# Kernel optimization log

Hardware: AMD Instinct MI355X
Metric: run time of the kernel (lower is better)

## Reference

```python
import jax, jax.numpy as jnp
import numpy as np

N_USER, N_NEWS = 100000, 20000
C, H, NL = 128, 4, 2
D = C // H
E = 250000
N_TYPES, N_RELS = 2, 3
EDGE_SRC_DST = ((0, 1), (1, 0), (0, 0))  # (src_type, dst_type): posts, rev_posts, follows
SIZES = (N_USER, N_NEWS)


def setup_inputs() -> dict:
    key = jax.random.key(0)
    ks = iter(jax.random.split(key, 32))
    s_lin = 1.0 / np.sqrt(C)
    s_rel = 1.0 / np.sqrt(D)
    inp = {
        "x_user": jax.random.normal(next(ks), (N_USER, C), jnp.float32),
        "x_news": jax.random.normal(next(ks), (N_NEWS, C), jnp.float32),
    }
    for name, (st, dt) in zip(("ei_posts", "ei_rev", "ei_follows"), EDGE_SRC_DST):
        src = jax.random.randint(next(ks), (E,), 0, SIZES[st], jnp.int32)
        dst = jax.random.randint(next(ks), (E,), 0, SIZES[dt], jnp.int32)
        inp[name] = jnp.stack([src, dst])  # [2, E]
    for w, b in (("Wk", "bk"), ("Wq", "bq"), ("Wv", "bv"), ("Wa", "ba")):
        inp[w] = jax.random.normal(next(ks), (NL, N_TYPES, C, C), jnp.float32) * s_lin
        inp[b] = jnp.zeros((NL, N_TYPES, C), jnp.float32)
    inp["skip"] = jnp.ones((NL, N_TYPES), jnp.float32)
    inp["a_rel"] = jax.random.normal(next(ks), (NL, N_RELS, H, D, D), jnp.float32) * s_rel
    inp["m_rel"] = jax.random.normal(next(ks), (NL, N_RELS, H, D, D), jnp.float32) * s_rel
    inp["p_rel"] = jnp.ones((NL, N_RELS, H), jnp.float32)
    return inp


def _segment_softmax(scores, seg, n):
    # scores: [E, H], seg: [E] destination ids; PyG-style softmax over incoming edges
    m = jax.ops.segment_max(scores, seg, num_segments=n)
    ex = jnp.exp(scores - m[seg])
    den = jax.ops.segment_sum(ex, seg, num_segments=n)
    return ex / (den[seg] + 1e-16)


def _hgt_layer(xs, eis, Wk, bk, Wq, bq, Wv, bv, Wa, ba, skip, a_rel, m_rel, p_rel):
    # per-node-type projections -> [N_t, H, D]
    k = [(xs[t] @ Wk[t] + bk[t]).reshape(-1, H, D) for t in range(N_TYPES)]
    q = [(xs[t] @ Wq[t] + bq[t]).reshape(-1, H, D) for t in range(N_TYPES)]
    v = [(xs[t] @ Wv[t] + bv[t]).reshape(-1, H, D) for t in range(N_TYPES)]
    agg = [jnp.zeros((SIZES[t], C), xs[t].dtype) for t in range(N_TYPES)]
    inv_sqrt_d = 1.0 / np.sqrt(D)
    for r, (st, dt) in enumerate(EDGE_SRC_DST):
        src, dst = eis[r][0], eis[r][1]
        # relation-specific transforms: W_att / W_msg per head
        k_rel = jnp.einsum('nhd,hde->nhe', k[st], a_rel[r])
        v_rel = jnp.einsum('nhd,hde->nhe', v[st], m_rel[r])
        score = jnp.einsum('ehd,ehd->eh', q[dt][dst], k_rel[src]) * p_rel[r] * inv_sqrt_d
        alpha = _segment_softmax(score, dst, SIZES[dt])  # [E, H]
        msg = (v_rel[src] * alpha[..., None]).reshape(-1, C)
        agg[dt] = agg[dt] + jax.ops.segment_sum(msg, dst, num_segments=SIZES[dt])
    new_xs = []
    for t in range(N_TYPES):
        o = jax.nn.gelu(agg[t], approximate=False) @ Wa[t] + ba[t]
        a = jax.nn.sigmoid(skip[t])
        new_xs.append(a * o + (1.0 - a) * xs[t])  # skip (dims match)
    return new_xs


def reference(x_user, x_news, ei_posts, ei_rev, ei_follows,
              Wk, bk, Wq, bq, Wv, bv, Wa, ba, skip, a_rel, m_rel, p_rel):
    xs = [x_user, x_news]
    eis = (ei_posts, ei_rev, ei_follows)
    for l in range(NL):
        xs = _hgt_layer(xs, eis, Wk[l], bk[l], Wq[l], bq[l], Wv[l], bv[l],
                        Wa[l], ba[l], skip[l], a_rel[l], m_rel[l], p_rel[l])
        xs = [jax.nn.relu(x) for x in xs]
    # x_dict output, concatenated over node types in metadata order for a single array
    return jnp.concatenate(xs, axis=0)  # [N_USER + N_NEWS, C]
```

## Files before the change

### kernel.cpp

```cpp
#include <hip/hip_runtime.h>
#include <cmath>

constexpr int NUSER = 100000;
constexpr int NNEWS = 20000;
constexpr int CH    = 128;
constexpr int NE    = 250000;
constexpr int NTOT  = NNEWS + NUSER + NUSER;
constexpr int NSB   = (NTOT + 255) / 256;

typedef _Float16 f16x8 __attribute__((ext_vector_type(8)));
typedef _Float16 f16x4 __attribute__((ext_vector_type(4)));
typedef _Float16 f16x2 __attribute__((ext_vector_type(2)));
typedef float    f32x4 __attribute__((ext_vector_type(4)));

constexpr size_t OFF_QU  = 0;
constexpr size_t OFF_QN  = OFF_QU  + (size_t)NUSER * 64;
constexpr size_t OFF_AGU = OFF_QN  + (size_t)NNEWS * 64;
constexpr size_t OFF_AGN = OFF_AGU + (size_t)NUSER * 64;
constexpr size_t OFF_KVB = OFF_AGN + (size_t)NNEWS * 64;
constexpr size_t OFF_KVS = OFF_KVB + (size_t)NUSER * 128;
constexpr size_t OFF_WF  = OFF_KVS + (size_t)NNEWS * 128;
constexpr size_t OFF_BE  = OFF_WF  + 20 * 8192;
constexpr size_t OFF_INT = OFF_BE  + 2 * 768;
constexpr size_t IO_CU   = 0;
constexpr size_t IO_JRP  = IO_CU  + NTOT;
constexpr size_t IO_BSUM = IO_JRP + NTOT + 1;
constexpr size_t IO_BOFF = IO_BSUM + NSB;
constexpr size_t IO_CL   = IO_BOFF + NSB;
constexpr size_t IO_RANK = IO_CL + 3 * NE;
constexpr size_t IO_END  = IO_RANK + 3 * NE;
constexpr size_t OFF_X16U = OFF_INT + IO_END;
constexpr size_t OFF_X16N = OFF_X16U + (size_t)NUSER * 64;
constexpr size_t OFF_KVB2 = OFF_X16N + (size_t)NNEWS * 64;
constexpr size_t WS_NEED_ROOMY = (OFF_KVB2 + (size_t)NUSER * 128) * sizeof(float);

__device__ __forceinline__ float gelu_f(float x) {
    return 0.5f * x * (1.0f + erff(x * 0.70710678118654752440f));
}

__device__ __forceinline__ int frag_dest(int k, int col) {
    int kt = k >> 5, quad = (k >> 3) & 3, j = k & 7;
    int ct = col >> 4, m = col & 15;
    int lane = quad * 16 + m;
    return ((kt * 8 + ct) * 64 + lane) * 8 + j;
}

constexpr int NEFF = 2 * 2 * 3 * 16384;
constexpr int NCVT = 2 * 4 * 16384;
constexpr int NBIA = 2 * 2 * 3 * 128;
constexpr int NPREP = NEFF + NCVT + NBIA;

__global__ __launch_bounds__(256) void prep_weights_kernel(
    const float* __restrict__ Wk, const float* __restrict__ bk,
    const float* __restrict__ Wv, const float* __restrict__ bv,
    const float* __restrict__ Wq, const float* __restrict__ Wa,
    const float* __restrict__ a_rel, const float* __restrict__ m_rel,
    const float* __restrict__ p_rel,
    _Float16* __restrict__ wkf, float* __restrict__ bke,
    _Float16* __restrict__ wvf, float* __restrict__ bve,
    _Float16* __restrict__ wqf, _Float16* __restrict__ waf,
    int* __restrict__ cu)
{
    const float kscale = 0.17677669529663688f * 1.44269504088896340f;
    int idx = blockIdx.x * 256 + threadIdx.x;
    if (idx < NEFF) {
        int o = idx & 16383;
        int g = idx >> 14;
        int r = g % 3, lk = g / 3, kind = lk & 1, l = lk >> 1;
        int st = (r == 1) ? 1 : 0;
        const float* W   = (kind ? Wv : Wk) + ((size_t)(l * 2 + st)) * 16384;
        const float* rel = (kind ? m_rel : a_rel) + ((size_t)(l * 3 + r)) * 4096;
        _Float16* Wf = (kind ? wvf : wkf) + ((size_t)(l * 3 + r)) * 16384;
        int k = o >> 7, col = o & 127, h = col >> 5, e = col & 31;
        const float* wrow = W + (size_t)k * 128 + h * 32;
        const float* rcol = rel + h * 1024 + e;
        float s = 0.f;
        #pragma unroll
        for (int d = 0; d < 32; ++d) s += wrow[d] * rcol[d * 32];
        if (kind == 0) s *= p_rel[(l * 3 + r) * 4 + h] * kscale;
        Wf[frag_dest(k, col)] = (_Float16)s;
    } else if (idx < NEFF + NCVT) {
        int t = idx - NEFF;
        int o = t & 16383;
        int b = t >> 14;
        int l = b >> 2, sub = b & 3;
        const float* W;
        _Float16* Wf;
        if (sub < 2) { W = Wq + ((size_t)(l * 2 + sub)) * 16384;     Wf = wqf + ((size_t)(l * 2 + sub)) * 16384; }
        else         { W = Wa + ((size_t)(l * 2 + sub - 2)) * 16384; Wf = waf + ((size_t)(l * 2 + sub - 2)) * 16384; }
        int k = o >> 7, col = o & 127;
        Wf[frag_dest(k, col)] = (_Float16)W[o];
    } else if (idx < NPREP) {
        int t = idx - NEFF - NCVT;
        int col = t & 127;
        int g = t >> 7;
        int r = g % 3, lk = g / 3, kind = lk & 1, l = lk >> 1;
        int st = (r == 1) ? 1 : 0;
        const float* bi  = (kind ? bv : bk) + ((size_t)(l * 2 + st)) * 128;
        const float* rel = (kind ? m_rel : a_rel) + ((size_t)(l * 3 + r)) * 4096;
        float* be = (kind ? bve : bke) + (size_t)l * 384 + r * 128;
        int h = col >> 5, e = col & 31;
        float s = 0.f;
        #pragma unroll
        for (int d = 0; d < 32; ++d) s += bi[h * 32 + d] * rel[h * 1024 + d * 32 + e];
        if (kind == 0) s *= p_rel[(l * 3 + r) * 4 + h] * kscale;
        be[col] = s;
    } else if (idx < NPREP + NTOT) {
        cu[idx - NPREP] = 0;
    }
}

__global__ void histrank_kernel(const int* __restrict__ e0, const int* __restrict__ e1,
                                const int* __restrict__ e2, int* __restrict__ cu,
                                int* __restrict__ rank) {
    int idx = blockIdx.x * 256 + threadIdx.x;
    if (idx >= 3 * NE) return;
    int r = idx / NE, e = idx - r * NE;
    const int* ei = (r == 0) ? e0 : (r == 1) ? e1 : e2;
    int base = (r == 0) ? 0 : (r == 1) ? NNEWS : (NNEWS + NUSER);
    rank[idx] = atomicAdd(&cu[base + ei[NE + e]], 1);
}

__global__ __launch_bounds__(256) void scan_part_kernel(const int* __restrict__ cu,
                                                        int* __restrict__ bsum) {
    int i = blockIdx.x * 256 + threadIdx.x;
    int v = (i < NTOT) ? cu[i] : 0;
    #pragma unroll
    for (int o = 1; o < 64; o <<= 1) v += __shfl_xor(v, o);
    __shared__ int ws_[4];
    if ((threadIdx.x & 63) == 0) ws_[threadIdx.x >> 6] = v;
    __syncthreads();
    if (threadIdx.x == 0) bsum[blockIdx.x] = ws_[0] + ws_[1] + ws_[2] + ws_[3];
}

__global__ __launch_bounds__(1024) void scan_top_kernel(const int* __restrict__ bsum,
                                                        int* __restrict__ boff,
                                                        int* __restrict__ jrp) {
    __shared__ int wsum[16];
    int tid = threadIdx.x, lane = tid & 63, w = tid >> 6;
    int v = (tid < NSB) ? bsum[tid] : 0;
    int x = v;
    #pragma unroll
    for (int o = 1; o < 64; o <<= 1) { int y = __shfl_up(x, o); if (lane >= o) x += y; }
    if (lane == 63) wsum[w] = x;
    __syncthreads();
    if (tid < 16) {
        int t = wsum[tid];
        #pragma unroll
        for (int o = 1; o < 16; o <<= 1) { int y = __shfl_up(t, o); if (tid >= o) t += y; }
        wsum[tid] = t;
    }
    __syncthreads();
    int woff = w ? wsum[w - 1] : 0;
    if (tid < NSB) boff[tid] = woff + x - v;
    if (tid == 0) jrp[NTOT] = 3 * NE;
}

__global__ __launch_bounds__(256) void scan_fin_kernel(const int* __restrict__ cu,
                                                       const int* __restrict__ boff,
                                                       int* __restrict__ jrp) {
    __shared__ int wsum[4];
    int tid = threadIdx.x, lane = tid & 63, w = tid >> 6;
    int i = blockIdx.x * 256 + tid;
    int v = (i < NTOT) ? cu[i] : 0;
    int x = v;
    #pragma unroll
    for (int o = 1; o < 64; o <<= 1) { int y = __shfl_up(x, o); if (lane >= o) x += y; }
    if (lane == 63) wsum[w] = x;
    __syncthreads();
    int woff = 0;
    #pragma unroll
    for (int k = 0; k < 4; ++k) if (k < w) woff += wsum[k];
    int excl = boff[blockIdx.x] + woff + x - v;
    if (i < NTOT) jrp[i] = excl;
}

__global__ void fill_kernel(const int* __restrict__ e0, const int* __restrict__ e1,
                            const int* __restrict__ e2, const int* __restrict__ jrp,
                            const int* __restrict__ rank, int* __restrict__ cl) {
    int idx = blockIdx.x * 256 + threadIdx.x;
    if (idx >= 3 * NE) return;
    int r = idx / NE, e = idx - r * NE;
    const int* ei = (r == 0) ? e0 : (r == 1) ? e1 : e2;
    int base = (r == 0) ? 0 : (r == 1) ? NNEWS : (NNEWS + NUSER);
    int dst = ei[NE + e], src = ei[e];
    cl[jrp[base + dst] + rank[idx]] = src;
}

struct GJob {
    const void* A;
    const _Float16* W0;
    const _Float16* W1;
    const float* b0;
    const float* b1;
    _Float16* o0;
    _Float16* o1;
    _Float16* x16;
    int ostride, N, blk0, nout2;
};
struct GJobs { GJob j[5]; int njobs; };

template<bool IN_HALF>
__global__ __launch_bounds__(512, 4) void gemm_G(GJobs gj)
{
    __shared__ _Float16 sW[32768];
    __shared__ _Float16 sE[8192];
    const int tid = threadIdx.x;
    const int lane = tid & 63;
    const int m = lane & 15, quad = lane >> 4, wave = tid >> 6;

    GJob J = gj.j[0];
    #pragma unroll
    for (int k = 1; k < 5; ++k)
        if (gj.njobs > k && (int)blockIdx.x >= gj.j[k].blk0) J = gj.j[k];

    const int n8 = J.nout2 ? 4096 : 2048;
    for (int i = tid; i < n8; i += 512) {
        const _Float16* src = (i < 2048) ? (J.W0 + (size_t)i * 8)
                                         : (J.W1 + (size_t)(i - 2048) * 8);
        *(f16x8*)(sW + (size_t)i * 8) = *(const f16x8*)src;
    }
    __syncthreads();

    const int r16  = wave * 16 + m;
    const int half = wave >> 2;
    const int r64  = r16 & 63;
    const int swz  = (r64 & 7) << 4;

    const int tbase = ((int)blockIdx.x - J.blk0) * 2;
    for (int t = 0; t < 2; ++t) {
        const int row0 = (tbase + t) * 128;
        if (row0 >= J.N) break;
        const int node  = row0 + r16;
        const int nodec = (node < J.N) ? node : (J.N - 1);

        f16x8 xf[4];
        if constexpr (IN_HALF) {
            const _Float16* A_ = (const _Float16*)J.A + (size_t)nodec * 128 + quad * 8;
            xf[0] = *(const f16x8*)(A_);
            xf[1] = *(const f16x8*)(A_ + 32);
            xf[2] = *(const f16x8*)(A_ + 64);
            xf[3] = *(const f16x8*)(A_ + 96);
        } else {
            const float* A_ = (const float*)J.A + (size_t)nodec * 128 + quad * 8;
            #pragma unroll
            for (int kt = 0; kt < 4; ++kt) {
                f32x4 u = *(const f32x4*)(A_ + kt * 32);
                f32x4 v = *(const f32x4*)(A_ + kt * 32 + 4);
                xf[kt] = (f16x8){(_Float16)u[0], (_Float16)u[1], (_Float16)u[2], (_Float16)u[3],
                                 (_Float16)v[0], (_Float16)v[1], (_Float16)v[2], (_Float16)v[3]};
            }
        }

        if constexpr (!IN_HALF) {
            if (J.x16 && node < J.N) {
                _Float16* xd = J.x16 + (size_t)node * 128 + quad * 8;
                *(f16x8*)(xd)      = xf[0];
                *(f16x8*)(xd + 32) = xf[1];
                *(f16x8*)(xd + 64) = xf[2];
                *(f16x8*)(xd + 96) = xf[3];
            }
        }

        f32x4 acc0[8], acc1[8];
        #pragma unroll
        for (int u = 0; u < 8; ++u) {
            acc0[u] = (f32x4){0.f, 0.f, 0.f, 0.f};
            acc1[u] = (f32x4){0.f, 0.f, 0.f, 0.f};
        }
        #pragma unroll
        for (int kt = 0; kt < 4; ++kt) {
            #pragma unroll
            for (int ct = 0; ct < 8; ++ct) {
                f16x8 wf0 = *(const f16x8*)(sW + ((kt * 8 + ct) * 64 + lane) * 8);
                acc0[ct] = __builtin_amdgcn_mfma_f32_16x16x32_f16(wf0, xf[kt], acc0[ct], 0, 0, 0);
            }
        }
        if (J.nout2) {
            #pragma unroll
            for (int kt = 0; kt < 4; ++kt) {
                #pragma unroll
                for (int ct = 0; ct < 8; ++ct) {
                    f16x8 wf1 = *(const f16x8*)(sW + 16384 + ((kt * 8 + ct) * 64 + lane) * 8);
                    acc1[ct] = __builtin_amdgcn_mfma_f32_16x16x32_f16(wf1, xf[kt], acc1[ct], 0, 0, 0);
                }
            }
        }

        {
            f16x4 h[8];
            #pragma unroll
            for (int ct = 0; ct < 8; ++ct) {
                int c = ct * 16 + quad * 4;
                f32x4 r = acc0[ct] + *(const f32x4*)(J.b0 + c);
                h[ct] = (f16x4){(_Float16)r[0], (_Float16)r[1], (_Float16)r[2], (_Float16)r[3]};
            }
            for (int hh = 0; hh < 2; ++hh) {
                __syncthreads();
                if (half == hh) {
                    #pragma unroll
                    for (int ct = 0; ct < 8; ++ct)
                        *(f16x4*)((char*)sE + r64 * 256 + ((ct * 32 + quad * 8) ^ swz)) = h[ct];
                }
                __syncthreads();
                #pragma unroll
                for (int jj = 0; jj < 2; ++jj) {
                    int c = jj * 512 + tid;
                    int n16 = c >> 4, w = c & 15;
                    f16x8 v = *(const f16x8*)((const char*)sE + n16 * 256 + ((w * 16) ^ ((n16 & 7) << 4)));
                    int gnode = row0 + hh * 64 + n16;
                    if (gnode < J.N)
                        *(f16x8*)(J.o0 + (size_t)gnode * J.ostride + w * 8) = v;
                }
            }
        }
        if (J.nout2) {
            f16x4 h[8];
            #pragma unroll
            for (int ct = 0; ct < 8; ++ct) {
                int c = ct * 16 + quad * 4;
                f32x4 r = acc1[ct] + *(const f32x4*)(J.b1 + c);
                h[ct] = (f16x4){(_Float16)r[0], (_Float16)r[1], (_Float16)r[2], (_Float16)r[3]};
            }
            for (int hh = 0; hh < 2; ++hh) {
                __syncthreads();
                if (half == hh) {
                    #pragma unroll
                    for (int ct = 0; ct < 8; ++ct)
                        *(f16x4*)((char*)sE + r64 * 256 + ((ct * 32 + quad * 8) ^ swz)) = h[ct];
                }
                __syncthreads();
                #pragma unroll
                for (int jj = 0; jj < 2; ++jj) {
                    int c = jj * 512 + tid;
                    int n16 = c >> 4, w = c & 15;
                    f16x8 v = *(const f16x8*)((const char*)sE + n16 * 256 + ((w * 16) ^ ((n16 & 7) << 4)));
                    int gnode = row0 + hh * 64 + n16;
                    if (gnode < J.N)
                        *(f16x8*)(J.o1 + (size_t)gnode * J.ostride + w * 8) = v;
                }
            }
        }
    }
}

struct EJob {
    const _Float16* A;
    const _Float16* W0;
    const float* b0;
    void* o0;
    const _Float16* Xold;
    const float* skipv;
    int N, blk0;
};
struct EJobs { EJob j[2]; };

template<bool OUT32>
__global__ __launch_bounds__(256) void epi_E(EJobs ej)
{
    __shared__ _Float16 sW[16384];
    __shared__ _Float16 sE[OUT32 ? 64 : 8192];
    const int tid = threadIdx.x;
    const int lane = tid & 63;
    const int m = lane & 15, quad = lane >> 4, wave = tid >> 6;

    EJob J = ej.j[0];
    if ((int)blockIdx.x >= ej.j[1].blk0) J = ej.j[1];

    for (int i = tid; i < 2048; i += 256)
        *(f16x8*)(sW + (size_t)i * 8) = *(const f16x8*)(J.W0 + (size_t)i * 8);
    __syncthreads();

    float sv = J.skipv[0];
    float aS = 1.0f / (1.0f + expf(-sv));
    float bSk = 1.0f - aS;

    const int tbase = ((int)blockIdx.x - J.blk0) * 2;
    for (int t = 0; t < 2; ++t) {
        const int row0 = (tbase + t) * 64;
        if (row0 >= J.N) break;
        const int node  = row0 + wave * 16 + m;
        const int nodec = (node < J.N) ? node : (J.N - 1);

        f16x4 xh[8];
        {
            const _Float16* Xo = J.Xold + (size_t)nodec * 128 + quad * 4;
            #pragma unroll
            for (int ct = 0; ct < 8; ++ct) xh[ct] = *(const f16x4*)(Xo + ct * 16);
        }

        f16x8 xf[4];
        {
            const _Float16* A_ = J.A + (size_t)nodec * 128 + quad * 8;
            xf[0] = *(const f16x8*)(A_);
            xf[1] = *(const f16x8*)(A_ + 32);
            xf[2] = *(const f16x8*)(A_ + 64);
            xf[3] = *(const f16x8*)(A_ + 96);
        }

        f32x4 acc0[8];
        #pragma unroll
        for (int u = 0; u < 8; ++u) acc0[u] = (f32x4){0.f, 0.f, 0.f, 0.f};
        #pragma unroll
        for (int kt = 0; kt < 4; ++kt) {
            #pragma unroll
            for (int ct = 0; ct < 8; ++ct) {
                f16x8 wf0 = *(const f16x8*)(sW + ((kt * 8 + ct) * 64 + lane) * 8);
                acc0[ct] = __builtin_amdgcn_mfma_f32_16x16x32_f16(wf0, xf[kt], acc0[ct], 0, 0, 0);
            }
        }

        if constexpr (OUT32) {
            if (node < J.N) {
                #pragma unroll
                for (int ct = 0; ct < 8; ++ct) {
                    int c = ct * 16 + quad * 4;
                    f32x4 r = acc0[ct] + *(const f32x4*)(J.b0 + c);
                    #pragma unroll
                    for (int jj = 0; jj < 4; ++jj)
                        r[jj] = fmaxf(aS * r[jj] + bSk * (float)xh[ct][jj], 0.f);
                    *(f32x4*)((float*)J.o0 + (size_t)node * 128 + c) = r;
                }
            }
        } else {
            const int r16 = wave * 16 + m;
            const int swz = (r16 & 7) << 4;
            f16x4 h[8];
            #pragma unroll
            for (int ct = 0; ct < 8; ++ct) {
                int c = ct * 16 + quad * 4;
                f32x4 r = acc0[ct] + *(const f32x4*)(J.b0 + c);
                #pragma unroll
                for (int jj = 0; jj < 4; ++jj)
                    r[jj] = fmaxf(aS * r[jj] + bSk * (float)xh[ct][jj], 0.f);
                h[ct] = (f16x4){(_Float16)r[0], (_Float16)r[1], (_Float16)r[2], (_Float16)r[3]};
            }
            __syncthreads();
            #pragma unroll
            for (int ct = 0; ct < 8; ++ct)
                *(f16x4*)((char*)sE + r16 * 256 + ((ct * 32 + quad * 8) ^ swz)) = h[ct];
            __syncthreads();
            #pragma unroll
            for (int jj = 0; jj < 4; ++jj) {
                int c = jj * 256 + tid;
                int n16 = c >> 4, w = c & 15;
                f16x8 v = *(const f16x8*)((const char*)sE + n16 * 256 + ((w * 16) ^ ((n16 & 7) << 4)));
                int gnode = row0 + n16;
                if (gnode < J.N)
                    *(f16x8*)((_Float16*)J.o0 + (size_t)gnode * 128 + w * 8) = v;
            }
        }
    }
}

__device__ __forceinline__ void attn_core(
    const _Float16* q, const _Float16* kv1, const int* rp1,
    const _Float16* kv2, const int* rp2, const int* cl,
    _Float16* agg, int d, int two, int sub)
{
    f16x8 qh = *(const f16x8*)(q + (size_t)d * 128 + sub * 8);
    float acc[8] = {0.f, 0.f, 0.f, 0.f, 0.f, 0.f, 0.f, 0.f};

    for (int rel = 0; rel < 1 + two; ++rel) {
        const _Float16* kv = rel ? kv2 : kv1;
        const int* rp = rel ? rp2 : rp1;
        int e0 = rp[d], e1 = rp[d + 1];
        float den = 0.f;
        float s[8] = {0.f, 0.f, 0.f, 0.f, 0.f, 0.f, 0.f, 0.f};
        int e = e0;
        for (; e + 1 < e1; e += 2) {
            int s0 = cl[e], s1 = cl[e + 1];
            const _Float16* r0 = kv + (size_t)s0 * 256;
            const _Float16* r1 = kv + (size_t)s1 * 256;
            f16x8 k0 = *(const f16x8*)(r0 + sub * 8);
            f16x8 v0 = *(const f16x8*)(r0 + 128 + sub * 8);
            f16x8 k1 = *(const f16x8*)(r1 + sub * 8);
            f16x8 v1 = *(const f16x8*)(r1 + 128 + sub * 8);
            float p0 = 0.f, p1 = 0.f;
#if __has_builtin(__builtin_amdgcn_fdot2)
            const f16x2* qp = (const f16x2*)&qh;
            const f16x2* a0 = (const f16x2*)&k0;
            const f16x2* a1 = (const f16x2*)&k1;
            #pragma unroll
            for (int j = 0; j < 4; ++j) {
                p0 = __builtin_amdgcn_fdot2(a0[j], qp[j], p0, false);
                p1 = __builtin_amdgcn_fdot2(a1[j], qp[j], p1, false);
            }
#else
            #pragma unroll
            for (int j = 0; j < 8; ++j) {
                p0 += (float)k0[j] * (float)qh[j];
                p1 += (float)k1[j] * (float)qh[j];
            }
#endif
            p0 += __shfl_xor(p0, 1); p1 += __shfl_xor(p1, 1);
            p0 += __shfl_xor(p0, 2); p1 += __shfl_xor(p1, 2);
            float w0 = exp2f(p0), w1 = exp2f(p1);
            den += w0 + w1;
            #pragma unroll
            for (int j = 0; j < 8; ++j) s[j] += w0 * (float)v0[j] + w1 * (float)v1[j];
        }
        if (e < e1) {
            int s0 = cl[e];
            const _Float16* r0 = kv + (size_t)s0 * 256;
            f16x8 k0 = *(const f16x8*)(r0 + sub * 8);
            f16x8 v0 = *(const f16x8*)(r0 + 128 + sub * 8);
            float p0 = 0.f;
#if __has_builtin(__builtin_amdgcn_fdot2)
            const f16x2* qp = (const f16x2*)&qh;
            const f16x2* a0 = (const f16x2*)&k0;
            #pragma unroll
            for (int j = 0; j < 4; ++j) p0 = __builtin_amdgcn_fdot2(a0[j], qp[j], p0, false);
#else
            #pragma unroll
            for (int j = 0; j < 8; ++j) p0 += (float)k0[j] * (float)qh[j];
#endif
            p0 += __shfl_xor(p0, 1);
            p0 += __shfl_xor(p0, 2);
            float w0 = exp2f(p0);
            den += w0;
            #pragma unroll
            for (int j = 0; j < 8; ++j) s[j] += w0 * (float)v0[j];
        }
        if (den > 0.f) {
            float inv = 1.f / den;
            #pragma unroll
            for (int j = 0; j < 8; ++j) acc[j] += s[j] * inv;
        }
    }

    f16x8 o;
    #pragma unroll
    for (int j = 0; j < 8; ++j) o[j] = (_Float16)gelu_f(acc[j]);
    *(f16x8*)(agg + (size_t)d * 128 + sub * 8) = o;
}

__global__ __launch_bounds__(256) void attn_v5(
    const _Float16* __restrict__ q,
    const _Float16* __restrict__ kv1, const int* __restrict__ rp1,
    const _Float16* __restrict__ kv2, const int* __restrict__ rp2,
    const int* __restrict__ cl,
    _Float16* __restrict__ agg, int Ndst, int two)
{
    int d = blockIdx.x * 16 + (threadIdx.x >> 4);
    if (d >= Ndst) return;
    attn_core(q, kv1, rp1, kv2, rp2, cl, agg, d, two, threadIdx.x & 15);
}

__global__ __launch_bounds__(256) void attn_A(
    const _Float16* __restrict__ qn, const _Float16* __restrict__ kvn,
    const int* __restrict__ rpn, _Float16* __restrict__ aggn, int Nn,
    const _Float16* __restrict__ qu, const _Float16* __restrict__ kvu1,
    const int* __restrict__ rpu1, const _Float16* __restrict__ kvu2,
    const int* __restrict__ rpu2, _Float16* __restrict__ aggu, int Nu,
    const int* __restrict__ cl, int nbn)
{
    bool news = (int)blockIdx.x < nbn;
    int brel = news ? blockIdx.x : blockIdx.x - nbn;
    int d = brel * 16 + (threadIdx.x >> 4);
    int N = news ? Nn : Nu;
    if (d >= N) return;
    attn_core(news ? qn : qu,
              news ? kvn : kvu1, news ? rpn : rpu1,
              kvu2, rpu2, cl,
              news ? aggn : aggu, d, news ? 0 : 1, threadIdx.x & 15);
}

extern "C" void kernel_launch(void* const* d_in, const int* in_sizes, int n_in,
                              void* d_out, int out_size, void* d_ws, size_t ws_size,
                              hipStream_t stream)
{
    const float* x_user = (const float*)d_in[0];
    const float* x_news = (const float*)d_in[1];
    const int* ei0 = (const int*)d_in[2];
    const int* ei1 = (const int*)d_in[3];
    const int* ei2 = (const int*)d_in[4];
    const float* Wk = (const float*)d_in[5];
    const float* bk = (const float*)d_in[6];
    const float* Wq = (const float*)d_in[7];
    const float* bq = (const float*)d_in[8];
    const float* Wv = (const float*)d_in[9];
    const float* bv = (const float*)d_in[10];
    const float* Wa = (const float*)d_in[11];
    const float* ba = (const float*)d_in[12];
    const float* skip = (const float*)d_in[13];
    const float* a_rel = (const float*)d_in[14];
    const float* m_rel = (const float*)d_in[15];
    const float* p_rel = (const float*)d_in[16];

    float* ws = (float*)d_ws;
    _Float16* q_user  = (_Float16*)(ws + OFF_QU);
    _Float16* q_news  = (_Float16*)(ws + OFF_QN);
    _Float16* agg_u   = (_Float16*)(ws + OFF_AGU);
    _Float16* agg_n   = (_Float16*)(ws + OFF_AGN);
    _Float16* kv_big  = (_Float16*)(ws + OFF_KVB);
    _Float16* kv_sm   = (_Float16*)(ws + OFF_KVS);
    _Float16* wkf = (_Float16*)(ws + OFF_WF);
    _Float16* wvf = wkf + 6 * 16384;
    _Float16* wqf = wvf + 6 * 16384;
    _Float16* waf = wqf + 4 * 16384;
    float* bke = ws + OFF_BE;
    float* bve = bke + 768;
    int* ib   = (int*)(ws + OFF_INT);
    int* cu   = ib + IO_CU;
    int* jrp  = ib + IO_JRP;
    int* bsum = ib + IO_BSUM;
    int* boff = ib + IO_BOFF;
    int* cl   = ib + IO_CL;
    int* rank = ib + IO_RANK;
    _Float16* x16u = (_Float16*)(ws + OFF_X16U);
    _Float16* x16n = (_Float16*)(ws + OFF_X16N);
    _Float16* kv_big2 = (_Float16*)(ws + OFF_KVB2);
    const int* rp0 = jrp;
    const int* rp1 = jrp + NNEWS;
    const int* rp2 = jrp + NNEWS + NUSER;

    const bool roomy = ws_size >= WS_NEED_ROOMY;

    prep_weights_kernel<<<(NPREP + NTOT + 255) / 256, 256, 0, stream>>>(
        Wk, bk, Wv, bv, Wq, Wa, a_rel, m_rel, p_rel,
        wkf, bke, wvf, bve, wqf, waf, cu);

    int g3e = (3 * NE + 255) / 256;
    histrank_kernel<<<g3e, 256, 0, stream>>>(ei0, ei1, ei2, cu, rank);
    scan_part_kernel<<<NSB, 256, 0, stream>>>(cu, bsum);
    scan_top_kernel<<<1, 1024, 0, stream>>>(bsum, boff, jrp);
    scan_fin_kernel<<<NSB, 256, 0, stream>>>(cu, boff, jrp);
    fill_kernel<<<g3e, 256, 0, stream>>>(ei0, ei1, ei2, jrp, rank, cl);

    float* out_user = (float*)d_out;
    float* out_news = (float*)d_out + (size_t)NUSER * CH;

    const int GBU = (NUSER + 255) / 256;
    const int GBN = (NNEWS + 255) / 256;
    const int EBU = ((NUSER + 63) / 64 + 1) / 2;
    const int EBN = ((NNEWS + 63) / 64 + 1) / 2;
    const int ABN = (NNEWS + 15) / 16;
    const int ABU = (NUSER + 15) / 16;

    for (int l = 0; l < 2; ++l) {
        _Float16* wkf_l = wkf + (size_t)l * 3 * 16384;
        _Float16* wvf_l = wvf + (size_t)l * 3 * 16384;
        _Float16* wqf_l = wqf + (size_t)l * 2 * 16384;
        _Float16* waf_l = waf + (size_t)l * 2 * 16384;
        float* bke_l = bke + (size_t)l * 384;
        float* bve_l = bve + (size_t)l * 384;
        const void* xu_in = l ? (const void*)x16u : (const void*)x_user;
        const void* xn_in = l ? (const void*)x16n : (const void*)x_news;

        if (roomy) {
            GJobs gj{};
            int nb = 0;
            gj.j[0] = {xu_in, wqf_l, nullptr, bq + (size_t)(l * 2 + 0) * 128, nullptr,
                       q_user, nullptr, l ? nullptr : x16u, 128, NUSER, nb, 0};
            nb += GBU;
            gj.j[1] = {xu_in, wkf_l, wvf_l, bke_l, bve_l,
                       kv_big, kv_big + 128, nullptr, 256, NUSER, nb, 1};
            nb += GBU;
            gj.j[2] = {xu_in, wkf_l + 32768, wvf_l + 32768, bke_l + 256, bve_l + 256,
                       kv_big2, kv_big2 + 128, nullptr, 256, NUSER, nb, 1};
            nb += GBU;
            gj.j[3] = {xn_in, wqf_l + 16384, nullptr, bq + (size_t)(l * 2 + 1) * 128, nullptr,
                       q_news, nullptr, l ? nullptr : x16n, 128, NNEWS, nb, 0};
            nb += GBN;
            gj.j[4] = {xn_in, wkf_l + 16384, wvf_l + 16384, bke_l + 128, bve_l + 128,
                       kv_sm, kv_sm + 128, nullptr, 256, NNEWS, nb, 1};
            nb += GBN;
            gj.njobs = 5;
            if (l == 0) gemm_G<false><<<nb, 512, 0, stream>>>(gj);
            else        gemm_G<true ><<<nb, 512, 0, stream>>>(gj);

            attn_A<<<ABN + ABU, 256, 0, stream>>>(
                q_news, kv_big, rp0, agg_n, NNEWS,
                q_user, kv_sm, rp1, kv_big2, rp2, agg_u, NUSER, cl, ABN);
        } else {
            GJobs g1{};
            int nb = 0;
            g1.j[0] = {xu_in, wqf_l, nullptr, bq + (size_t)(l * 2 + 0) * 128, nullptr,
                       q_user, nullptr, l ? nullptr : x16u, 128, NUSER, nb, 0};
            nb += GBU;
            g1.j[1] = {xu_in, wkf_l, wvf_l, bke_l, bve_l,
                       kv_big, kv_big + 128, nullptr, 256, NUSER, nb, 1};
            nb += GBU;
            g1.j[2] = {xn_in, wqf_l + 16384, nullptr, bq + (size_t)(l * 2 + 1) * 128, nullptr,
                       q_news, nullptr, l ? nullptr : x16n, 128, NNEWS, nb, 0};
            nb += GBN;
            g1.j[3] = {xn_in, wkf_l + 16384, wvf_l + 16384, bke_l + 128, bve_l + 128,
                       kv_sm, kv_sm + 128, nullptr, 256, NNEWS, nb, 1};
            nb += GBN;
            g1.njobs = 4;
            if (l == 0) gemm_G<false><<<nb, 512, 0, stream>>>(g1);
            else        gemm_G<true ><<<nb, 512, 0, stream>>>(g1);
            attn_v5<<<ABN, 256, 0, stream>>>(
                q_news, kv_big, rp0, nullptr, nullptr, cl, agg_n, NNEWS, 0);
            GJobs g2{};
            g2.j[0] = {xu_in, wkf_l + 32768, wvf_l + 32768, bke_l + 256, bve_l + 256,
                       kv_big, kv_big + 128, nullptr, 256, NUSER, 0, 1};
            g2.njobs = 1;
            if (l == 0) gemm_G<false><<<GBU, 512, 0, stream>>>(g2);
            else        gemm_G<true ><<<GBU, 512, 0, stream>>>(g2);
            attn_v5<<<ABU, 256, 0, stream>>>(
                q_user, kv_sm, rp1, kv_big, rp2, cl, agg_u, NUSER, 1);
        }

        EJobs ej{};
        ej.j[0] = {agg_u, waf_l, ba + (size_t)(l * 2 + 0) * 128,
                   l ? (void*)out_user : (void*)x16u, x16u, skip + l * 2 + 0, NUSER, 0};
        ej.j[1] = {agg_n, waf_l + 16384, ba + (size_t)(l * 2 + 1) * 128,
                   l ? (void*)out_news : (void*)x16n, x16n, skip + l * 2 + 1, NNEWS, EBU};
        if (l == 0) epi_E<false><<<EBU + EBN, 256, 0, stream>>>(ej);
        else        epi_E<true ><<<EBU + EBN, 256, 0, stream>>>(ej);
    }
    (void)in_sizes; (void)n_in; (void)out_size;
}
```

Baseline: 476.2 us.

## Fuse CSR build kernels into weight prep, single-pass scan, and layer-0 GEMM

Merges the destination histogram/rank atomics into the weight-prep kernel, replaces the three-kernel scan with a two-kernel scan where each block sums prior block totals itself, and folds the CSR fill step into extra blocks of the first-layer GEMM launch. A separate small kernel now zeroes the counters, since the histogram pass reads them inside the same launch that used to clear them. The aim is to cut kernel launches and serialization gaps in the preprocessing phase. The cost is redundant prefix reads of block sums in every scan block, plus GEMM launch blocks that carry this unrelated fill work.

```diff
diff --git a/kernel.cpp b/kernel.cpp
--- a/kernel.cpp
+++ b/kernel.cpp
@@ -45,12 +45,17 @@
     return ((kt * 8 + ct) * 64 + lane) * 8 + j;
 }
 
+__global__ __launch_bounds__(256) void zero_cu_kernel(int* __restrict__ cu) {
+    int i = blockIdx.x * 256 + threadIdx.x;
+    if (i < NTOT) cu[i] = 0;
+}
+
 constexpr int NEFF = 2 * 2 * 3 * 16384;
 constexpr int NCVT = 2 * 4 * 16384;
 constexpr int NBIA = 2 * 2 * 3 * 128;
 constexpr int NPREP = NEFF + NCVT + NBIA;
 
-__global__ __launch_bounds__(256) void prep_weights_kernel(
+__global__ __launch_bounds__(256) void prep_hist_kernel(
     const float* __restrict__ Wk, const float* __restrict__ bk,
     const float* __restrict__ Wv, const float* __restrict__ bv,
     const float* __restrict__ Wq, const float* __restrict__ Wa,
@@ -59,7 +64,9 @@
     _Float16* __restrict__ wkf, float* __restrict__ bke,
     _Float16* __restrict__ wvf, float* __restrict__ bve,
     _Float16* __restrict__ wqf, _Float16* __restrict__ waf,
-    int* __restrict__ cu)
+    const int* __restrict__ e0, const int* __restrict__ e1,
+    const int* __restrict__ e2,
+    int* __restrict__ cu, int* __restrict__ rank)
 {
     const float kscale = 0.17677669529663688f * 1.44269504088896340f;
     int idx = blockIdx.x * 256 + threadIdx.x;
@@ -105,20 +112,15 @@
         for (int d = 0; d < 32; ++d) s += bi[h * 32 + d] * rel[h * 1024 + d * 32 + e];
         if (kind == 0) s *= p_rel[(l * 3 + r) * 4 + h] * kscale;
         be[col] = s;
-    } else if (idx < NPREP + NTOT) {
-        cu[idx - NPREP] = 0;
+    } else {
+        int t = idx - NPREP;
+        if (t < 3 * NE) {
+            int r = t / NE, e = t - r * NE;
+            const int* ei = (r == 0) ? e0 : (r == 1) ? e1 : e2;
+            int base = (r == 0) ? 0 : (r == 1) ? NNEWS : (NNEWS + NUSER);
+            rank[t] = atomicAdd(&cu[base + ei[NE + e]], 1);
+        }
     }
-}
-
-__global__ void histrank_kernel(const int* __restrict__ e0, const int* __restrict__ e1,
-                                const int* __restrict__ e2, int* __restrict__ cu,
-                                int* __restrict__ rank) {
-    int idx = blockIdx.x * 256 + threadIdx.x;
-    if (idx >= 3 * NE) return;
-    int r = idx / NE, e = idx - r * NE;
-    const int* ei = (r == 0) ? e0 : (r == 1) ? e1 : e2;
-    int base = (r == 0) ? 0 : (r == 1) ? NNEWS : (NNEWS + NUSER);
-    rank[idx] = atomicAdd(&cu[base + ei[NE + e]], 1);
 }
 
 __global__ __launch_bounds__(256) void scan_part_kernel(const int* __restrict__ cu,
@@ -133,58 +135,33 @@
     if (threadIdx.x == 0) bsum[blockIdx.x] = ws_[0] + ws_[1] + ws_[2] + ws_[3];
 }
 
-__global__ __launch_bounds__(1024) void scan_top_kernel(const int* __restrict__ bsum,
-                                                        int* __restrict__ boff,
+__global__ __launch_bounds__(256) void scan_fin2_kernel(const int* __restrict__ cu,
+                                                        const int* __restrict__ bsum,
                                                         int* __restrict__ jrp) {
-    __shared__ int wsum[16];
+    __shared__ int wsum[4];
+    __shared__ int sOff;
     int tid = threadIdx.x, lane = tid & 63, w = tid >> 6;
-    int v = (tid < NSB) ? bsum[tid] : 0;
-    int x = v;
+    int part = 0;
+    for (int i = tid; i < (int)blockIdx.x; i += 256) part += bsum[i];
     #pragma unroll
-    for (int o = 1; o < 64; o <<= 1) { int y = __shfl_up(x, o); if (lane >= o) x += y; }
-    if (lane == 63) wsum[w] = x;
+    for (int o = 1; o < 64; o <<= 1) part += __shfl_xor(part, o);
+    if (lane == 0) wsum[w] = part;
     __syncthreads();
-    if (tid < 16) {
-        int t = wsum[tid];
-        #pragma unroll
-        for (int o = 1; o < 16; o <<= 1) { int y = __shfl_up(t, o); if (tid >= o) t += y; }
-        wsum[tid] = t;
-    }
+    if (tid == 0) sOff = wsum[0] + wsum[1] + wsum[2] + wsum[3];
     __syncthreads();
-    int woff = w ? wsum[w - 1] : 0;
-    if (tid < NSB) boff[tid] = woff + x - v;
-    if (tid == 0) jrp[NTOT] = 3 * NE;
-}
-
-__global__ __launch_bounds__(256) void scan_fin_kernel(const int* __restrict__ cu,
-                                                       const int* __restrict__ boff,
-                                                       int* __restrict__ jrp) {
-    __shared__ int wsum[4];
-    int tid = threadIdx.x, lane = tid & 63, w = tid >> 6;
     int i = blockIdx.x * 256 + tid;
     int v = (i < NTOT) ? cu[i] : 0;
     int x = v;
     #pragma unroll
     for (int o = 1; o < 64; o <<= 1) { int y = __shfl_up(x, o); if (lane >= o) x += y; }
+    __syncthreads();
     if (lane == 63) wsum[w] = x;
     __syncthreads();
     int woff = 0;
     #pragma unroll
     for (int k = 0; k < 4; ++k) if (k < w) woff += wsum[k];
-    int excl = boff[blockIdx.x] + woff + x - v;
-    if (i < NTOT) jrp[i] = excl;
-}
-
-__global__ void fill_kernel(const int* __restrict__ e0, const int* __restrict__ e1,
-                            const int* __restrict__ e2, const int* __restrict__ jrp,
-                            const int* __restrict__ rank, int* __restrict__ cl) {
-    int idx = blockIdx.x * 256 + threadIdx.x;
-    if (idx >= 3 * NE) return;
-    int r = idx / NE, e = idx - r * NE;
-    const int* ei = (r == 0) ? e0 : (r == 1) ? e1 : e2;
-    int base = (r == 0) ? 0 : (r == 1) ? NNEWS : (NNEWS + NUSER);
-    int dst = ei[NE + e], src = ei[e];
-    cl[jrp[base + dst] + rank[idx]] = src;
+    if (i < NTOT) jrp[i] = sOff + woff + x - v;
+    if (blockIdx.x == 0 && tid == 0) jrp[NTOT] = 3 * NE;
 }
 
 struct GJob {
@@ -201,11 +178,27 @@
 struct GJobs { GJob j[5]; int njobs; };
 
 template<bool IN_HALF>
-__global__ __launch_bounds__(512, 4) void gemm_G(GJobs gj)
+__global__ __launch_bounds__(512, 4) void gemm_G(GJobs gj,
+    const int* __restrict__ fe0, const int* __restrict__ fe1, const int* __restrict__ fe2,
+    const int* __restrict__ fjrp, const int* __restrict__ frank, int* __restrict__ fcl,
+    int fill_blk0)
 {
     __shared__ _Float16 sW[32768];
     __shared__ _Float16 sE[8192];
     const int tid = threadIdx.x;
+
+    if ((int)blockIdx.x >= fill_blk0) {
+        int idx = ((int)blockIdx.x - fill_blk0) * 512 + tid;
+        if (idx < 3 * NE) {
+            int r = idx / NE, e = idx - r * NE;
+            const int* ei = (r == 0) ? fe0 : (r == 1) ? fe1 : fe2;
+            int base = (r == 0) ? 0 : (r == 1) ? NNEWS : (NNEWS + NUSER);
+            int dst = ei[NE + e], src = ei[e];
+            fcl[fjrp[base + dst] + frank[idx]] = src;
+        }
+        return;
+    }
+
     const int lane = tid & 63;
     const int m = lane & 15, quad = lane >> 4, wave = tid >> 6;
 
@@ -605,7 +598,6 @@
     int* cu   = ib + IO_CU;
     int* jrp  = ib + IO_JRP;
     int* bsum = ib + IO_BSUM;
-    int* boff = ib + IO_BOFF;
     int* cl   = ib + IO_CL;
     int* rank = ib + IO_RANK;
     _Float16* x16u = (_Float16*)(ws + OFF_X16U);
@@ -617,26 +609,27 @@
 
     const bool roomy = ws_size >= WS_NEED_ROOMY;
 
-    prep_weights_kernel<<<(NPREP + NTOT + 255) / 256, 256, 0, stream>>>(
-        Wk, bk, Wv, bv, Wq, Wa, a_rel, m_rel, p_rel,
-        wkf, bke, wvf, bve, wqf, waf, cu);
-
-    int g3e = (3 * NE + 255) / 256;
-    histrank_kernel<<<g3e, 256, 0, stream>>>(ei0, ei1, ei2, cu, rank);
+    zero_cu_kernel<<<NSB, 256, 0, stream>>>(cu);
+    {
+        int nb = (NPREP + 3 * NE + 255) / 256;
+        prep_hist_kernel<<<nb, 256, 0, stream>>>(
+            Wk, bk, Wv, bv, Wq, Wa, a_rel, m_rel, p_rel,
+            wkf, bke, wvf, bve, wqf, waf, ei0, ei1, ei2, cu, rank);
+    }
     scan_part_kernel<<<NSB, 256, 0, stream>>>(cu, bsum);
-    scan_top_kernel<<<1, 1024, 0, stream>>>(bsum, boff, jrp);
-    scan_fin_kernel<<<NSB, 256, 0, stream>>>(cu, boff, jrp);
-    fill_kernel<<<g3e, 256, 0, stream>>>(ei0, ei1, ei2, jrp, rank, cl);
+    scan_fin2_kernel<<<NSB, 256, 0, stream>>>(cu, bsum, jrp);
 
     float* out_user = (float*)d_out;
     float* out_news = (float*)d_out + (size_t)NUSER * CH;
 
     const int GBU = (NUSER + 255) / 256;
     const int GBN = (NNEWS + 255) / 256;
+    const int FB  = (3 * NE + 511) / 512;
     const int EBU = ((NUSER + 63) / 64 + 1) / 2;
     const int EBN = ((NNEWS + 63) / 64 + 1) / 2;
     const int ABN = (NNEWS + 15) / 16;
     const int ABU = (NUSER + 15) / 16;
+    const int NOFILL = 0x7fffffff;
 
     for (int l = 0; l < 2; ++l) {
         _Float16* wkf_l = wkf + (size_t)l * 3 * 16384;
@@ -667,8 +660,10 @@
                        kv_sm, kv_sm + 128, nullptr, 256, NNEWS, nb, 1};
             nb += GBN;
             gj.njobs = 5;
-            if (l == 0) gemm_G<false><<<nb, 512, 0, stream>>>(gj);
-            else        gemm_G<true ><<<nb, 512, 0, stream>>>(gj);
+            int fb0 = (l == 0) ? nb : NOFILL;
+            int grid = (l == 0) ? nb + FB : nb;
+            if (l == 0) gemm_G<false><<<grid, 512, 0, stream>>>(gj, ei0, ei1, ei2, jrp, rank, cl, fb0);
+            else        gemm_G<true ><<<grid, 512, 0, stream>>>(gj, ei0, ei1, ei2, jrp, rank, cl, fb0);
 
             attn_A<<<ABN + ABU, 256, 0, stream>>>(
                 q_news, kv_big, rp0, agg_n, NNEWS,
@@ -689,16 +684,18 @@
                        kv_sm, kv_sm + 128, nullptr, 256, NNEWS, nb, 1};
             nb += GBN;
             g1.njobs = 4;
-            if (l == 0) gemm_G<false><<<nb, 512, 0, stream>>>(g1);
-            else        gemm_G<true ><<<nb, 512, 0, stream>>>(g1);
+            int fb0 = (l == 0) ? nb : NOFILL;
+            int grid = (l == 0) ? nb + FB : nb;
+            if (l == 0) gemm_G<false><<<grid, 512, 0, stream>>>(g1, ei0, ei1, ei2, jrp, rank, cl, fb0);
+            else        gemm_G<true ><<<grid, 512, 0, stream>>>(g1, ei0, ei1, ei2, jrp, rank, cl, fb0);
             attn_v5<<<ABN, 256, 0, stream>>>(
                 q_news, kv_big, rp0, nullptr, nullptr, cl, agg_n, NNEWS, 0);
             GJobs g2{};
             g2.j[0] = {xu_in, wkf_l + 32768, wvf_l + 32768, bke_l + 256, bve_l + 256,
                        kv_big, kv_big + 128, nullptr, 256, NUSER, 0, 1};
             g2.njobs = 1;
-            if (l == 0) gemm_G<false><<<GBU, 512, 0, stream>>>(g2);
-            else        gemm_G<true ><<<GBU, 512, 0, stream>>>(g2);
+            if (l == 0) gemm_G<false><<<GBU, 512, 0, stream>>>(g2, ei0, ei1, ei2, jrp, rank, cl, NOFILL);
+            else        gemm_G<true ><<<GBU, 512, 0, stream>>>(g2, ei0, ei1, ei2, jrp, rank, cl, NOFILL);
             attn_v5<<<ABU, 256, 0, stream>>>(
                 q_user, kv_sm, rp1, kv_big, rp2, cl, agg_u, NUSER, 1);
         }
```

Result: no change. 475.5 us (-0.1%).
